# Kernel optimization log

Measured on AMD Instinct MI355X. Metric: run time of the kernel, lower is better.

The kernel has to match this reference:

```python
import jax, jax.numpy as jnp
import numpy as np

NUM_CAPSULE = 16
DIM_CAPSULE = 16
NUM_ROUTING = 3
EPS = 1e-7  # K.epsilon()


def squash(v, axis=-1):
    s2 = jnp.sum(jnp.square(v), axis=axis, keepdims=True) + EPS
    scale = s2 / ((1.0 + s2) * jnp.sqrt(s2))
    return scale * v


def setup_inputs() -> dict:
    key = jax.random.key(0)
    k1, k2 = jax.random.split(key)
    B, N, IC, ID = 64, 128, 32, 8
    x = jax.random.normal(k1, (B, N, IC, ID), dtype=jnp.float32)
    # glorot_uniform for W: [IC, ID, NUM_CAPSULE*DIM_CAPSULE]
    fan_in, fan_out = ID, NUM_CAPSULE * DIM_CAPSULE
    limit = np.sqrt(6.0 / (fan_in + fan_out))
    W = jax.random.uniform(k2, (IC, ID, NUM_CAPSULE * DIM_CAPSULE), dtype=jnp.float32,
                           minval=-limit, maxval=limit)
    return {"x": x, "W": W}


def reference(x, W):
    B, N, IC, ID = x.shape
    NC, DC = NUM_CAPSULE, DIM_CAPSULE
    u = x.reshape(-1, IC, ID)  # [BN, IC, ID]
    # prediction vectors: [BN, IC, NC*DC] -> [BN, NC, IC, DC]
    u_hat = jnp.einsum('bij,ijk->bik', u, W).reshape(-1, IC, NC, DC).transpose(0, 2, 1, 3)
    u_hat_stopped = jax.lax.stop_gradient(u_hat)
    b = jnp.zeros((u_hat.shape[0], NC, IC), dtype=x.dtype)
    outputs = None
    for i in range(NUM_ROUTING):
        c = jax.nn.softmax(b, axis=1)  # softmax over num_capsule axis (dim=1 in source)
        hat = u_hat if i == NUM_ROUTING - 1 else u_hat_stopped
        outputs = squash(jnp.einsum('bci,bcid->bcd', c, hat))  # [BN, NC, DC]
        if i < NUM_ROUTING - 1:
            b = b + jnp.einsum('bcd,bcid->bci', outputs, u_hat_stopped)
    return outputs.reshape(B, N, NC, DC)
```

## Files before the change

### kernel.cpp

```cpp
#include <hip/hip_runtime.h>
#include <hip/hip_bf16.h>


#define S 2

typedef float    v2f __attribute__((ext_vector_type(2)));
typedef _Float16 v2h __attribute__((ext_vector_type(2)));

template <int CTRL>
__device__ __forceinline__ float dppf(float x) {
  return __builtin_bit_cast(float,
      __builtin_amdgcn_update_dpp(0, __builtin_bit_cast(int, x), CTRL, 0xF, 0xF, true));
}
template <int CTRL>
__device__ __forceinline__ v2f dpp2(v2f v) {
  v2f r;
  r.x = dppf<CTRL>(v.x);
  r.y = dppf<CTRL>(v.y);
  return r;
}
template <int CTRL, int BANK>
__device__ __forceinline__ float dpp_old(float old, float x) {
  return __builtin_bit_cast(float,
      __builtin_amdgcn_update_dpp(__builtin_bit_cast(int, old),
                                  __builtin_bit_cast(int, x), CTRL, 0xF, BANK, false));
}
__device__ __forceinline__ float xor4_recv(float lo , float hi ) {
  float ya = dpp_old<0x104, 0x5>(0.0f, lo);
  return dpp_old<0x114, 0xA>(ya, hi);
}

#if __has_builtin(__builtin_amdgcn_fdot2)
__device__ __forceinline__ float dot2(v2h a, v2h b, float c) {
  return __builtin_amdgcn_fdot2(a, b, c, false);
}
#else
__device__ __forceinline__ float dot2(v2h a, v2h b, float c) {
  return fmaf((float)a.x, (float)b.x, fmaf((float)a.y, (float)b.y, c));
}
#endif

__global__ __launch_bounds__(256) void prep_kernel(const float* __restrict__ W,
                                                   const float* __restrict__ x,
                                                   _Float16* __restrict__ Wth,
                                                   _Float16* __restrict__ xh) {
  int bid = blockIdx.x;
  if (bid < 256) {
    int o  = bid * 256 + threadIdx.x;
    int ic = o >> 11;
    int k  = (o >> 3) & 255;
    int id = o & 7;
    Wth[o] = (_Float16)W[(ic * 8 + id) * 256 + k];
  } else {
    int tid = (bid - 256) * 256 + threadIdx.x;
    const float4* xp = (const float4*)x + tid * 2;
    float4 f0 = xp[0], f1 = xp[1];
    v2h h0 = {(_Float16)f0.x, (_Float16)f0.y};
    v2h h1 = {(_Float16)f0.z, (_Float16)f0.w};
    v2h h2 = {(_Float16)f1.x, (_Float16)f1.y};
    v2h h3 = {(_Float16)f1.z, (_Float16)f1.w};
    uint4 o;
    o.x = __builtin_bit_cast(unsigned, h0);
    o.y = __builtin_bit_cast(unsigned, h1);
    o.z = __builtin_bit_cast(unsigned, h2);
    o.w = __builtin_bit_cast(unsigned, h3);
    ((uint4*)xh)[tid] = o;
  }
}

__device__ __forceinline__ v2f squash2(v2f o) {
  v2f s2 = o * o;
  s2 += dpp2<0xB1>(s2);
  s2 += dpp2<0x4E>(s2);
  s2 += dpp2<0x141>(s2);
  s2 += dpp2<0x140>(s2);
  s2 += (v2f){1e-7f, 1e-7f};
  v2f sc;
  sc.x = s2.x * __builtin_amdgcn_rsqf(s2.x) * __builtin_amdgcn_rcpf(1.f + s2.x);
  sc.y = s2.y * __builtin_amdgcn_rsqf(s2.y) * __builtin_amdgcn_rcpf(1.f + s2.y);
  return o * sc;
}

template <bool ASSIGN>
__device__ __forceinline__ void b_update2(v2f v, const v2f* uh2, int dc,
                                          float* bp0, float* bp1) {
#pragma unroll
  for (int icb = 0; icb < 32; icb += 16) {
    v2f a[16];
#pragma unroll
    for (int j = 0; j < 16; ++j) a[j] = v * uh2[icb + j];
    v2f b8[8];
    const bool u8 = (dc & 8) != 0;
#pragma unroll
    for (int j = 0; j < 8; ++j) {
      v2f send = u8 ? a[j] : a[j + 8];
      v2f recv = dpp2<0x128>(send);
      b8[j] = (u8 ? a[j + 8] : a[j]) + recv;
    }
    v2f c4[4];
    const bool u4 = (dc & 4) != 0;
#pragma unroll
    for (int j = 0; j < 4; ++j) {
      v2f recv;
      recv.x = xor4_recv(b8[j].x, b8[j + 4].x);
      recv.y = xor4_recv(b8[j].y, b8[j + 4].y);
      c4[j] = (u4 ? b8[j + 4] : b8[j]) + recv;
    }
    v2f d2[2];
    const bool u2 = (dc & 2) != 0;
#pragma unroll
    for (int j = 0; j < 2; ++j) {
      v2f send = u2 ? c4[j] : c4[j + 2];
      v2f recv = dpp2<0x4E>(send);
      d2[j] = (u2 ? c4[j + 2] : c4[j]) + recv;
    }
    const bool u1 = (dc & 1) != 0;
    v2f send = u1 ? d2[0] : d2[1];
    v2f recv = dpp2<0xB1>(send);
    v2f e = (u1 ? d2[1] : d2[0]) + recv;
    if (ASSIGN) { bp0[icb + dc] = e.x;  bp1[icb + dc] = e.y; }
    else        { bp0[icb + dc] += e.x; bp1[icb + dc] += e.y; }
  }
}

__global__ __launch_bounds__(256, 3) void caps_kernel(const _Float16* __restrict__ xh,
                                                      const uint4* __restrict__ Wt4,
                                                      float* __restrict__ out) {
  const int t  = threadIdx.x;
  const int nc = t >> 4;
  const int dc = t & 15;
  const int s0 = blockIdx.x * S;

  __shared__ float b_lds[S][16][33];
  __shared__ __align__(16) float c_lds[16][68];

  v2f uh2[32];
  v2f o2 = (v2f){0.f, 0.f};

  const v2h* xp0 = (const v2h*)(xh + (s0 + 0) * 256);
  const v2h* xp1 = (const v2h*)(xh + (s0 + 1) * 256);
#pragma unroll
  for (int ic = 0; ic < 32; ++ic) {
    uint4 wv = Wt4[ic * 256 + t];
    v2h w0 = __builtin_bit_cast(v2h, wv.x);
    v2h w1 = __builtin_bit_cast(v2h, wv.y);
    v2h w2 = __builtin_bit_cast(v2h, wv.z);
    v2h w3 = __builtin_bit_cast(v2h, wv.w);
    float a0 = dot2(xp0[ic * 4 + 3], w3,
               dot2(xp0[ic * 4 + 2], w2,
               dot2(xp0[ic * 4 + 1], w1,
               dot2(xp0[ic * 4 + 0], w0, 0.f))));
    float a1 = dot2(xp1[ic * 4 + 3], w3,
               dot2(xp1[ic * 4 + 2], w2,
               dot2(xp1[ic * 4 + 1], w1,
               dot2(xp1[ic * 4 + 0], w0, 0.f))));
    v2f u = (v2f){a0, a1};
    uh2[ic] = u;
    o2 += u;
  }

  {
    v2f v = squash2(o2 * (v2f){0.0625f, 0.0625f});
    b_update2<true>(v, uh2, dc, &b_lds[0][nc][0], &b_lds[1][nc][0]);
  }
  __syncthreads();

#pragma unroll
  for (int r = 1; r < 3; ++r) {
    {
      const int ss  = t >> 7;
      const int icc = (t >> 2) & 31;
      const int q   = t & 3;
      float e0 = __expf(b_lds[ss][4 * q + 0][icc]);
      float e1 = __expf(b_lds[ss][4 * q + 1][icc]);
      float e2 = __expf(b_lds[ss][4 * q + 2][icc]);
      float e3 = __expf(b_lds[ss][4 * q + 3][icc]);
      float ps = (e0 + e1) + (e2 + e3);
      ps += dppf<0xB1>(ps);
      ps += dppf<0x4E>(ps);
      float inv = __builtin_amdgcn_rcpf(ps);
      c_lds[4 * q + 0][2 * icc + ss] = e0 * inv;
      c_lds[4 * q + 1][2 * icc + ss] = e1 * inv;
      c_lds[4 * q + 2][2 * icc + ss] = e2 * inv;
      c_lds[4 * q + 3][2 * icc + ss] = e3 * inv;
    }
    __syncthreads();

    const float4* cp = (const float4*)&c_lds[nc][0];
    v2f o = (v2f){0.f, 0.f};
#pragma unroll
    for (int j = 0; j < 16; ++j) {
      float4 cc = cp[j];
      o = __builtin_elementwise_fma((v2f){cc.x, cc.y}, uh2[2 * j + 0], o);
      o = __builtin_elementwise_fma((v2f){cc.z, cc.w}, uh2[2 * j + 1], o);
    }
    v2f v = squash2(o);
    if (r == 2) {
      out[(s0 + 0) * 256 + t] = v.x;
      out[(s0 + 1) * 256 + t] = v.y;
    } else {
      b_update2<false>(v, uh2, dc, &b_lds[0][nc][0], &b_lds[1][nc][0]);
    }
    __syncthreads();
  }
}

extern "C" void kernel_launch(void* const* d_in, const int* in_sizes, int n_in,
                              void* d_out, int out_size, void* d_ws, size_t ws_size,
                              hipStream_t stream) {
  const float* x = (const float*)d_in[0];
  const float* W = (const float*)d_in[1];
  _Float16* Wth = (_Float16*)d_ws;
  _Float16* xh  = (_Float16*)d_ws + 65536;

  prep_kernel<<<1280, 256, 0, stream>>>(W, x, Wth, xh);
  caps_kernel<<<8192 / S, 256, 0, stream>>>(xh, (const uint4*)Wth, (float*)d_out);
}
```

Before: 98.08 us.

## Store prediction vectors and routing math in packed fp16, raise occupancy

Stores the u_hat prediction vectors as packed half2 instead of float2, and does the routing weighted sum and the b-update reduction in packed fp16 arithmetic. The routing coefficients go to LDS as fp16. Halving the register footprint lets launch bounds rise from 3 to 6 blocks per CU to improve latency hiding, and packed fp16 ops halve the DPP shuffle count. This costs accuracy, since sums and the agreement logits are accumulated in fp16, and it also drops the final barrier after the last iteration.

```diff
diff --git a/kernel.cpp b/kernel.cpp
--- a/kernel.cpp
+++ b/kernel.cpp
@@ -6,6 +6,10 @@
 
 typedef float    v2f __attribute__((ext_vector_type(2)));
 typedef _Float16 v2h __attribute__((ext_vector_type(2)));
+
+__device__ __forceinline__ v2h pack2h(float a, float b) {
+  return __builtin_bit_cast(v2h, __builtin_amdgcn_cvt_pkrtz(a, b));
+}
 
 template <int CTRL>
 __device__ __forceinline__ float dppf(float x) {
@@ -13,21 +17,18 @@
       __builtin_amdgcn_update_dpp(0, __builtin_bit_cast(int, x), CTRL, 0xF, 0xF, true));
 }
 template <int CTRL>
-__device__ __forceinline__ v2f dpp2(v2f v) {
-  v2f r;
-  r.x = dppf<CTRL>(v.x);
-  r.y = dppf<CTRL>(v.y);
-  return r;
+__device__ __forceinline__ v2h dpph(v2h v) {
+  return __builtin_bit_cast(v2h,
+      __builtin_amdgcn_update_dpp(0, __builtin_bit_cast(int, v), CTRL, 0xF, 0xF, true));
 }
 template <int CTRL, int BANK>
-__device__ __forceinline__ float dpp_old(float old, float x) {
-  return __builtin_bit_cast(float,
-      __builtin_amdgcn_update_dpp(__builtin_bit_cast(int, old),
-                                  __builtin_bit_cast(int, x), CTRL, 0xF, BANK, false));
-}
-__device__ __forceinline__ float xor4_recv(float lo , float hi ) {
-  float ya = dpp_old<0x104, 0x5>(0.0f, lo);
-  return dpp_old<0x114, 0xA>(ya, hi);
+__device__ __forceinline__ int dpp_old_i(int old, int x) {
+  return __builtin_amdgcn_update_dpp(old, x, CTRL, 0xF, BANK, false);
+}
+__device__ __forceinline__ v2h xor4t_h(v2h s) {
+  int si = __builtin_bit_cast(int, s);
+  int ya = dpp_old_i<0x104, 0x5>(0, si);
+  return __builtin_bit_cast(v2h, dpp_old_i<0x114, 0xA>(ya, si));
 }
 
 #if __has_builtin(__builtin_amdgcn_fdot2)
@@ -70,10 +71,10 @@
 
 __device__ __forceinline__ v2f squash2(v2f o) {
   v2f s2 = o * o;
-  s2 += dpp2<0xB1>(s2);
-  s2 += dpp2<0x4E>(s2);
-  s2 += dpp2<0x141>(s2);
-  s2 += dpp2<0x140>(s2);
+  s2.x += dppf<0xB1>(s2.x);   s2.y += dppf<0xB1>(s2.y);
+  s2.x += dppf<0x4E>(s2.x);   s2.y += dppf<0x4E>(s2.y);
+  s2.x += dppf<0x141>(s2.x);  s2.y += dppf<0x141>(s2.y);
+  s2.x += dppf<0x140>(s2.x);  s2.y += dppf<0x140>(s2.y);
   s2 += (v2f){1e-7f, 1e-7f};
   v2f sc;
   sc.x = s2.x * __builtin_amdgcn_rsqf(s2.x) * __builtin_amdgcn_rcpf(1.f + s2.x);
@@ -82,48 +83,50 @@
 }
 
 template <bool ASSIGN>
-__device__ __forceinline__ void b_update2(v2f v, const v2f* uh2, int dc,
+__device__ __forceinline__ void b_update2(v2h vh, const v2h* uh, int dc,
                                           float* bp0, float* bp1) {
 #pragma unroll
   for (int icb = 0; icb < 32; icb += 16) {
-    v2f a[16];
-#pragma unroll
-    for (int j = 0; j < 16; ++j) a[j] = v * uh2[icb + j];
-    v2f b8[8];
+    v2h a[16];
+#pragma unroll
+    for (int j = 0; j < 16; ++j) a[j] = vh * uh[icb + j];
+    v2h b8[8];
     const bool u8 = (dc & 8) != 0;
 #pragma unroll
     for (int j = 0; j < 8; ++j) {
-      v2f send = u8 ? a[j] : a[j + 8];
-      v2f recv = dpp2<0x128>(send);
+      v2h send = u8 ? a[j] : a[j + 8];
+      v2h recv = dpph<0x128>(send);
       b8[j] = (u8 ? a[j + 8] : a[j]) + recv;
     }
-    v2f c4[4];
+    v2h c4[4];
     const bool u4 = (dc & 4) != 0;
 #pragma unroll
     for (int j = 0; j < 4; ++j) {
-      v2f recv;
-      recv.x = xor4_recv(b8[j].x, b8[j + 4].x);
-      recv.y = xor4_recv(b8[j].y, b8[j + 4].y);
+      v2h send = u4 ? b8[j] : b8[j + 4];
+      v2h recv = xor4t_h(send);
       c4[j] = (u4 ? b8[j + 4] : b8[j]) + recv;
     }
-    v2f d2[2];
+    v2h d2[2];
     const bool u2 = (dc & 2) != 0;
 #pragma unroll
     for (int j = 0; j < 2; ++j) {
-      v2f send = u2 ? c4[j] : c4[j + 2];
-      v2f recv = dpp2<0x4E>(send);
+      v2h send = u2 ? c4[j] : c4[j + 2];
+      v2h recv = dpph<0x4E>(send);
       d2[j] = (u2 ? c4[j + 2] : c4[j]) + recv;
     }
     const bool u1 = (dc & 1) != 0;
-    v2f send = u1 ? d2[0] : d2[1];
-    v2f recv = dpp2<0xB1>(send);
-    v2f e = (u1 ? d2[1] : d2[0]) + recv;
-    if (ASSIGN) { bp0[icb + dc] = e.x;  bp1[icb + dc] = e.y; }
-    else        { bp0[icb + dc] += e.x; bp1[icb + dc] += e.y; }
-  }
-}
-
-__global__ __launch_bounds__(256, 3) void caps_kernel(const _Float16* __restrict__ xh,
+    v2h send = u1 ? d2[0] : d2[1];
+    v2h recv = dpph<0xB1>(send);
+    v2h e = (u1 ? d2[1] : d2[0]) + recv;
+    float e0 = (float)e.x, e1 = (float)e.y;
+    if (ASSIGN) { bp0[icb + dc] = e0;  bp1[icb + dc] = e1; }
+    else        { bp0[icb + dc] += e0; bp1[icb + dc] += e1; }
+  }
+}
+
+#define CSTRIDE 40
+
+__global__ __launch_bounds__(256, 6) void caps_kernel(const _Float16* __restrict__ xh,
                                                       const uint4* __restrict__ Wt4,
                                                       float* __restrict__ out) {
   const int t  = threadIdx.x;
@@ -132,9 +135,9 @@
   const int s0 = blockIdx.x * S;
 
   __shared__ float b_lds[S][16][33];
-  __shared__ __align__(16) float c_lds[16][68];
-
-  v2f uh2[32];
+  __shared__ v2h c16h[16 * CSTRIDE];
+
+  v2h uh[32];
   v2f o2 = (v2f){0.f, 0.f};
 
   const v2h* xp0 = (const v2h*)(xh + (s0 + 0) * 256);
@@ -154,14 +157,14 @@
                dot2(xp1[ic * 4 + 2], w2,
                dot2(xp1[ic * 4 + 1], w1,
                dot2(xp1[ic * 4 + 0], w0, 0.f))));
-    v2f u = (v2f){a0, a1};
-    uh2[ic] = u;
-    o2 += u;
+    o2 += (v2f){a0, a1};
+    uh[ic] = pack2h(a0, a1);
   }
 
   {
     v2f v = squash2(o2 * (v2f){0.0625f, 0.0625f});
-    b_update2<true>(v, uh2, dc, &b_lds[0][nc][0], &b_lds[1][nc][0]);
+    v2h vh = pack2h(v.x, v.y);
+    b_update2<true>(vh, uh, dc, &b_lds[0][nc][0], &b_lds[1][nc][0]);
   }
   __syncthreads();
 
@@ -179,29 +182,33 @@
       ps += dppf<0xB1>(ps);
       ps += dppf<0x4E>(ps);
       float inv = __builtin_amdgcn_rcpf(ps);
-      c_lds[4 * q + 0][2 * icc + ss] = e0 * inv;
-      c_lds[4 * q + 1][2 * icc + ss] = e1 * inv;
-      c_lds[4 * q + 2][2 * icc + ss] = e2 * inv;
-      c_lds[4 * q + 3][2 * icc + ss] = e3 * inv;
+      _Float16* cw = (_Float16*)c16h + ss;
+      cw[((4 * q + 0) * CSTRIDE + icc) * 2] = (_Float16)(e0 * inv);
+      cw[((4 * q + 1) * CSTRIDE + icc) * 2] = (_Float16)(e1 * inv);
+      cw[((4 * q + 2) * CSTRIDE + icc) * 2] = (_Float16)(e2 * inv);
+      cw[((4 * q + 3) * CSTRIDE + icc) * 2] = (_Float16)(e3 * inv);
     }
     __syncthreads();
 
-    const float4* cp = (const float4*)&c_lds[nc][0];
-    v2f o = (v2f){0.f, 0.f};
+    const v2h* crow = &c16h[nc * CSTRIDE];
+    v2h oh = (v2h){(_Float16)0.f, (_Float16)0.f};
 #pragma unroll
     for (int j = 0; j < 16; ++j) {
-      float4 cc = cp[j];
-      o = __builtin_elementwise_fma((v2f){cc.x, cc.y}, uh2[2 * j + 0], o);
-      o = __builtin_elementwise_fma((v2f){cc.z, cc.w}, uh2[2 * j + 1], o);
-    }
+      v2h cA = crow[j];
+      v2h cB = crow[j + 16];
+      oh = __builtin_elementwise_fma(cA, uh[j], oh);
+      oh = __builtin_elementwise_fma(cB, uh[16 + j], oh);
+    }
+    v2f o = (v2f){(float)oh.x, (float)oh.y};
     v2f v = squash2(o);
     if (r == 2) {
       out[(s0 + 0) * 256 + t] = v.x;
       out[(s0 + 1) * 256 + t] = v.y;
     } else {
-      b_update2<false>(v, uh2, dc, &b_lds[0][nc][0], &b_lds[1][nc][0]);
-    }
-    __syncthreads();
+      v2h vh = pack2h(v.x, v.y);
+      b_update2<false>(vh, uh, dc, &b_lds[0][nc][0], &b_lds[1][nc][0]);
+      __syncthreads();
+    }
   }
 }
 
```

New measurement: 91.30 us. 6.9% less time.
